# Kernel optimization log

Hardware: AMD Instinct MI355X
Metric: run time of the kernel (lower is better)

The kernel has to match this reference:

```python
import jax, jax.numpy as jnp
import numpy as np
from jax import lax

T, H, I, E = 1024, 1024, 512, 16          # tokens, hidden, moe_intermediate, n_routed_experts
TOP_K, N_GROUP, TOPK_GROUP = 4, 4, 2
N_SHARED = 2
I_SHARED = I * N_SHARED                    # shared-expert intermediate size
ROUTED_SCALE = 2.5


def setup_inputs() -> dict:
    key = jax.random.key(0)
    ks = jax.random.split(key, 9)
    s = lambda k, shape, fan: jax.random.normal(k, shape, jnp.float32) * (fan ** -0.5)
    return {
        "hidden_states": jax.random.normal(ks[0], (T, H), jnp.float32),
        "router_w": s(ks[1], (H, E), H),                 # gate: ReplicatedLinear(H, E)
        "e_bias": jax.random.normal(ks[2], (E,), jnp.float32) * 0.01,  # e_score_correction_bias
        "w_gate": s(ks[3], (E, H, I), H),                # routed experts gate_proj
        "w_up": s(ks[4], (E, H, I), H),                  # routed experts up_proj
        "w_down": s(ks[5], (E, I, H), I),                # routed experts down_proj
        "sw_gate": s(ks[6], (H, I_SHARED), H),           # shared experts gate_proj
        "sw_up": s(ks[7], (H, I_SHARED), H),             # shared experts up_proj
        "sw_down": s(ks[8], (I_SHARED, H), I_SHARED),    # shared experts down_proj
    }


def _grouped_topk_sigmoid(logits, e_bias):
    # DeepSeek-V3 'noaux_tc' grouped top-k with sigmoid scoring.
    scores = jax.nn.sigmoid(logits)                      # [T, E]
    sc = scores + e_bias                                 # biased scores for selection only
    g = sc.reshape(-1, N_GROUP, E // N_GROUP)
    group_scores = lax.top_k(g, 2)[0].sum(-1)            # [T, n_group]: sum of top-2 per group
    _, gidx = lax.top_k(group_scores, TOPK_GROUP)        # [T, topk_group]
    gmask = jax.nn.one_hot(gidx, N_GROUP, dtype=sc.dtype).sum(1)  # [T, n_group]
    emask = jnp.repeat(gmask, E // N_GROUP, axis=1)      # [T, E]
    masked = jnp.where(emask > 0, sc, 0.0)               # sigmoid scores are >=0
    _, tidx = lax.top_k(masked, TOP_K)                   # [T, top_k]
    w = jnp.take_along_axis(scores, tidx, axis=1)        # weights use UNbiased scores
    w = w / (w.sum(-1, keepdims=True) + 1e-20)           # norm_topk_prob=True
    # dense combine weights [T, E]
    combine = (jax.nn.one_hot(tidx, E, dtype=w.dtype) * w[..., None]).sum(1)
    return combine


def reference(hidden_states, router_w, e_bias, w_gate, w_up, w_down,
              sw_gate, sw_up, sw_down):
    x = hidden_states                                    # [T, H]
    logits = x @ router_w                                # [T, E]
    combine = _grouped_topk_sigmoid(logits, e_bias)      # [T, E]

    # routed experts: SiLU-gated MLP per expert, dense-over-experts reference
    gp = jnp.einsum('th,ehi->tei', x, w_gate)            # [T, E, I]
    up = jnp.einsum('th,ehi->tei', x, w_up)
    h = jax.nn.silu(gp) * up
    oe = jnp.einsum('tei,eih->teh', h, w_down)           # [T, E, H]
    routed = jnp.einsum('teh,te->th', oe, combine)       # [T, H]

    # shared experts MLP (reduce_results=False path), fp32 path scales routed only
    shared = (jax.nn.silu(x @ sw_gate) * (x @ sw_up)) @ sw_down  # [T, H]
    return routed * ROUTED_SCALE + shared
```

## Files before the change

### kernel.cpp

```cpp
#include <hip/hip_runtime.h>
#include <stdint.h>

#define T_TOK 1024
#define HDIM  1024
#define IDIM  512
#define NEXP  16
#define ISH   1024
#define MAXT128  48
#define HSLOTS   6144
#define NSCHED   (MAXT128 * 8)

typedef _Float16 f16;
typedef __attribute__((ext_vector_type(8))) _Float16 f16x8;
typedef __attribute__((ext_vector_type(4))) _Float16 f16x4;
typedef __attribute__((ext_vector_type(4))) float    f32x4;

__device__ __forceinline__ void gld16(const void* g, void* l) {
  __builtin_amdgcn_global_load_lds(
      (__attribute__((address_space(1))) void*)(uintptr_t)g,
      (__attribute__((address_space(3))) void*)(uint32_t)(uintptr_t)l,
      16, 0, 0);
}

__device__ __forceinline__ f16x8 ldsfragA(const f16* buf, int row, int lch) {
  int phys = lch ^ (row & 7);
  return *(const f16x8*)(buf + row * 64 + phys * 8);
}

__device__ __forceinline__ f16x8 ldsfragB(const f16* buf, int n, int kc) {
  int c = kc ^ ((n >> 3) & 7);
  return *(const f16x8*)(buf + n * 72 + c * 8);
}

__device__ __forceinline__ void loadB(const float* __restrict__ W, int ldW,
                                      int kt, int n0, int tid2, float2* v) {
  int p = tid2 & 31, kg = tid2 >> 5;
  const float* src = W + (size_t)(kt + 8 * kg) * ldW + n0 + 2 * p;
#pragma unroll
  for (int r = 0; r < 8; r++) v[r] = *(const float2*)(src + (size_t)r * ldW);
}
__device__ __forceinline__ void writeB(f16* __restrict__ Bs, int nbase, int tid2,
                                       const float2* v) {
  int p = tid2 & 31, kg = tid2 >> 5;
  f16x8 c0, c1;
#pragma unroll
  for (int r = 0; r < 8; r++) { c0[r] = (f16)v[r].x; c1[r] = (f16)v[r].y; }
  int nn = nbase + 2 * p;
  int cc = kg ^ ((nn >> 3) & 7);
  *(f16x8*)(Bs + (size_t)nn * 72 + cc * 8) = c0;
  *(f16x8*)(Bs + (size_t)(nn + 1) * 72 + cc * 8) = c1;
}

__global__ __launch_bounds__(256) void router_kernel(
    const float* __restrict__ x, const float* __restrict__ rw, const float* __restrict__ ebias,
    f16* __restrict__ xh, int* __restrict__ topk_i, float* __restrict__ topk_w) {
  int wave = threadIdx.x >> 6, l = threadIdx.x & 63;
  int t = blockIdx.x * 4 + wave;
  float acc[16];
#pragma unroll
  for (int e = 0; e < 16; e++) acc[e] = 0.f;
#pragma unroll
  for (int i = 0; i < 4; i++) {
    int k = i * 256 + l * 4;
    float4 xv = *(const float4*)(x + (size_t)t * HDIM + k);
    f16x4 h = { (f16)xv.x, (f16)xv.y, (f16)xv.z, (f16)xv.w };
    *(f16x4*)(xh + (size_t)t * HDIM + k) = h;
    const float* xp = &xv.x;
#pragma unroll
    for (int j = 0; j < 4; j++) {
      float xj = xp[j];
      const float4* w4 = (const float4*)(rw + (size_t)(k + j) * 16);
#pragma unroll
      for (int q = 0; q < 4; q++) {
        float4 w = w4[q];
        acc[q*4+0] += xj * w.x; acc[q*4+1] += xj * w.y;
        acc[q*4+2] += xj * w.z; acc[q*4+3] += xj * w.w;
      }
    }
  }
#pragma unroll
  for (int off = 32; off >= 1; off >>= 1)
#pragma unroll
    for (int e = 0; e < 16; e++) acc[e] += __shfl_xor(acc[e], off, 64);

  if (l == 0) {
    float s[16], sc[16];
#pragma unroll
    for (int e = 0; e < 16; e++) {
      s[e] = 1.f / (1.f + __expf(-acc[e]));
      sc[e] = s[e] + ebias[e];
    }
    float gs[4];
#pragma unroll
    for (int g = 0; g < 4; g++) {
      float a = -1e30f, b2 = -1e30f;
#pragma unroll
      for (int j = 0; j < 4; j++) {
        float v = sc[g*4 + j];
        if (v > a) { b2 = a; a = v; } else if (v > b2) { b2 = v; }
      }
      gs[g] = a + b2;
    }
    int g1 = 0;
    for (int g = 1; g < 4; g++) if (gs[g] > gs[g1]) g1 = g;
    int g2 = -1;
    for (int g = 0; g < 4; g++) if (g != g1 && (g2 < 0 || gs[g] > gs[g2])) g2 = g;
    float masked[16];
#pragma unroll
    for (int e = 0; e < 16; e++) {
      int g = e >> 2;
      masked[e] = (g == g1 || g == g2) ? sc[e] : 0.0f;
    }
    int idx[4]; float wv[4]; float denom = 1e-20f;
#pragma unroll
    for (int j = 0; j < 4; j++) {
      int best = 0; float bv = masked[0];
      for (int e = 1; e < 16; e++) if (masked[e] > bv) { bv = masked[e]; best = e; }
      idx[j] = best; wv[j] = s[best]; denom += s[best];
      masked[best] = -1e30f;
    }
#pragma unroll
    for (int j = 0; j < 4; j++) {
      topk_i[t * 4 + j] = idx[j];
      topk_w[t * 4 + j] = wv[j] / denom * 2.5f;
    }
  }
}

__global__ __launch_bounds__(1024) void scatter_kernel(
    const int* __restrict__ tki,
    int* __restrict__ tok, int* __restrict__ slotmap,
    int* __restrict__ tile_e, int* __restrict__ tile_srow,
    int* __restrict__ tile_hb, int* __restrict__ ntl, int* __restrict__ sched) {
  __shared__ int lcnt[NEXP], lpos[NEXP], lbase[NEXP];
  int t = threadIdx.x;
  if (t < NEXP) { lcnt[t] = 0; lpos[t] = 0; }
  if (t < NSCHED) sched[t] = -1;
  __syncthreads();
  int idx[4];
#pragma unroll
  for (int j = 0; j < 4; j++) idx[j] = tki[t*4+j];
#pragma unroll
  for (int j = 0; j < 4; j++) atomicAdd(&lcnt[idx[j]], 1);
  __syncthreads();
  if (t == 0) {
    int total = 0, slots = 0;
    int sc[8];
    for (int q = 0; q < 8; q++) sc[q] = 0;
    for (int e = 0; e < NEXP; e++) {
      int c = lcnt[e], nt = (c + 127) >> 7;
      lbase[e] = slots;
      for (int j = 0; j < nt; j++) {
        tile_e[total] = e; tile_srow[total] = j * 128; tile_hb[total] = slots + j * 128;
        int x = e & 7;
        if (sc[x] + 8 > MAXT128) {
          int bx = 0;
          for (int q = 1; q < 8; q++) if (sc[q] < sc[bx]) bx = q;
          x = bx;
        }
        for (int n = 0; n < 8; n++) { sched[x + 8 * sc[x]] = total * 8 + n; sc[x]++; }
        total++;
      }
      slots += nt * 128;
    }
    ntl[0] = total;
  }
  __syncthreads();
#pragma unroll
  for (int j = 0; j < 4; j++) {
    int slot = atomicAdd(&lpos[idx[j]], 1);
    tok[idx[j] * T_TOK + slot] = t;
    slotmap[t * 4 + j] = lbase[idx[j]] + slot;
  }
  __syncthreads();
  int e = t >> 6, s = t & 63;
  int c = lcnt[e];
  int top = ((c + 127) >> 7) << 7;
  for (int s2 = c + s; s2 < top; s2 += 64) tok[e * T_TOK + s2] = 0;
}

__device__ __forceinline__ f32x4 mfma16(f16x8 a, f16x8 b, f32x4 c) {
  return __builtin_amdgcn_mfma_f32_16x16x32_f16(a, b, c, 0, 0, 0);
}

__global__ __launch_bounds__(512, 4) void gu_all(
    const f16* __restrict__ xh,
    const float* __restrict__ sg, const float* __restrict__ su, f16* __restrict__ hsh,
    const float* __restrict__ wg, const float* __restrict__ wu, f16* __restrict__ hbuf,
    const int* __restrict__ tile_e, const int* __restrict__ tile_srow,
    const int* __restrict__ tile_hb, const int* __restrict__ ntl,
    const int* __restrict__ tok, const int* __restrict__ sched) {
  int b = blockIdx.x;
  const float *Bg, *Bu; f16* Hdst;
  int e = 0, srow = 0, mbase, n0, N;
  bool gather = (b >= 128);
  if (!gather) {
    int x = b & 7, s = b >> 3;
    Bg = sg; Bu = su; Hdst = hsh; N = ISH;
    mbase = (s >> 1) * 128;
    n0 = (x + ((s & 1) << 3)) * 64;
  } else {
    int w = sched[b - 128];
    if (w < 0) return;
    int by = w >> 3;
    e = tile_e[by]; srow = tile_srow[by]; mbase = tile_hb[by];
    size_t bo = (size_t)e * HDIM * IDIM;
    Bg = wg + bo; Bu = wu + bo; Hdst = hbuf; N = IDIM;
    n0 = (w & 7) * 64;
  }
  const int K = HDIM;

  __shared__ f16 As[2 * 128 * 64];
  __shared__ f16 Bgs[2 * 64 * 72], Bus[2 * 64 * 72];

  int tid = threadIdx.x, lane = tid & 63, wave = tid >> 6;
  int quad = lane >> 4, l15 = lane & 15;
  int r = lane >> 3, p = lane & 7;

  const f16* gbA[2]; f16* lbA[2];
#pragma unroll
  for (int jj = 0; jj < 2; jj++) {
    int j = wave * 2 + jj;
    int kcol = (p ^ r) << 3;
    int row = j * 8 + r;
    int grow = gather ? tok[e * T_TOK + srow + row] : (mbase + row);
    gbA[jj] = xh + (size_t)grow * K + kcol;
    lbA[jj] = (f16*)As + (j << 9);
  }

  const float* Bmine = (tid < 256) ? Bg : Bu;
  f16* Bsmine = (tid < 256) ? (f16*)Bgs : (f16*)Bus;
  int tid2 = tid & 255;

  int wr = wave >> 1, wc = wave & 1;
  f32x4 zero = {0.f, 0.f, 0.f, 0.f};
  f32x4 aG[2][2], aU[2][2];
#pragma unroll
  for (int mi = 0; mi < 2; mi++)
#pragma unroll
    for (int ni = 0; ni < 2; ni++) { aG[mi][ni] = zero; aU[mi][ni] = zero; }

  float2 v[8];
#pragma unroll
  for (int jj = 0; jj < 2; jj++) gld16(gbA[jj], lbA[jj]);
  loadB(Bmine, N, 0, n0, tid2, v);
  writeB(Bsmine, 0, tid2, v);
  __syncthreads();

  const int nk = K >> 6;
  for (int it = 0; it < nk; ++it) {
    int cb = it & 1, nb = cb ^ 1;
    bool pf = (it + 1 < nk);
    if (pf) {
      int kt = (it + 1) << 6;
#pragma unroll
      for (int jj = 0; jj < 2; jj++) gld16(gbA[jj] + kt, lbA[jj] + nb * 8192);
      loadB(Bmine, N, kt, n0, tid2, v);
    }
    const f16* Ab = (const f16*)As + cb * 8192;
    const f16* Gb = (const f16*)Bgs + cb * 4608;
    const f16* Ub = (const f16*)Bus + cb * 4608;
#pragma unroll
    for (int ks = 0; ks < 2; ks++) {
      int lch = (ks << 2) + quad;
      f16x8 a[2], g[2], u[2];
#pragma unroll
      for (int mi = 0; mi < 2; mi++) a[mi] = ldsfragA(Ab, 32 * wr + 16 * mi + l15, lch);
#pragma unroll
      for (int ni = 0; ni < 2; ni++) {
        g[ni] = ldsfragB(Gb, 32 * wc + 16 * ni + l15, lch);
        u[ni] = ldsfragB(Ub, 32 * wc + 16 * ni + l15, lch);
      }
#pragma unroll
      for (int mi = 0; mi < 2; mi++)
#pragma unroll
        for (int ni = 0; ni < 2; ni++) {
          aG[mi][ni] = mfma16(a[mi], g[ni], aG[mi][ni]);
          aU[mi][ni] = mfma16(a[mi], u[ni], aU[mi][ni]);
        }
    }
    if (pf) writeB(Bsmine + nb * 4608, 0, tid2, v);
    __syncthreads();
  }
#pragma unroll
  for (int mi = 0; mi < 2; mi++)
#pragma unroll
    for (int ni = 0; ni < 2; ni++)
#pragma unroll
      for (int rg = 0; rg < 4; rg++) {
        int m = 32 * wr + 16 * mi + (quad << 2) + rg;
        int n = n0 + 32 * wc + 16 * ni + l15;
        float g = aG[mi][ni][rg], u = aU[mi][ni][rg];
        float val = (g / (1.f + __expf(-g))) * u;
        Hdst[(size_t)(mbase + m) * N + n] = (f16)val;
      }
}

__global__ __launch_bounds__(512, 4) void down_all(
    const f16* __restrict__ hsh, const float* __restrict__ sd,
    const f16* __restrict__ hbuf, const float* __restrict__ wd,
    float* __restrict__ out, f16* __restrict__ odown,
    const int* __restrict__ tile_hb, const int* __restrict__ tile_e,
    const int* __restrict__ ntl, const int* __restrict__ sched) {
  int b = blockIdx.x;
  bool routed = (b >= 64);
  const f16* A; const float* B; int K, abase, n0;
  if (!routed) {
    A = hsh; B = sd; K = ISH;
    n0 = (b & 7) * 128; abase = (b >> 3) * 128;
  } else {
    int w = sched[b - 64];
    if (w < 0) return;
    int by = w >> 3;
    abase = tile_hb[by];
    A = hbuf; B = wd + (size_t)tile_e[by] * IDIM * HDIM; K = IDIM;
    n0 = (w & 7) * 128;
  }

  __shared__ f16 As[2 * 128 * 64];
  __shared__ f16 Bs[2 * 128 * 72];

  int tid = threadIdx.x, lane = tid & 63, wave = tid >> 6;
  int quad = lane >> 4, l15 = lane & 15;
  int r = lane >> 3, p = lane & 7;

  const f16* gbA[2]; f16* lbA[2];
#pragma unroll
  for (int jj = 0; jj < 2; jj++) {
    int j = wave * 2 + jj;
    int kcol = (p ^ r) << 3;
    int row = j * 8 + r;
    gbA[jj] = A + (size_t)(abase + row) * K + kcol;
    lbA[jj] = (f16*)As + (j << 9);
  }

  int nb0 = (tid < 256) ? 0 : 64;
  int tid2 = tid & 255;

  int wr = wave >> 1, wc = wave & 1;
  f32x4 zero = {0.f, 0.f, 0.f, 0.f};
  f32x4 ac[2][4];
#pragma unroll
  for (int mi = 0; mi < 2; mi++)
#pragma unroll
    for (int ni = 0; ni < 4; ni++) ac[mi][ni] = zero;

  float2 v[8];
#pragma unroll
  for (int jj = 0; jj < 2; jj++) gld16(gbA[jj], lbA[jj]);
  loadB(B, HDIM, 0, n0 + nb0, tid2, v);
  writeB((f16*)Bs, nb0, tid2, v);
  __syncthreads();

  const int nk = K >> 6;
  for (int it = 0; it < nk; ++it) {
    int cb = it & 1, nb = cb ^ 1;
    bool pf = (it + 1 < nk);
    if (pf) {
      int kt = (it + 1) << 6;
#pragma unroll
      for (int jj = 0; jj < 2; jj++) gld16(gbA[jj] + kt, lbA[jj] + nb * 8192);
      loadB(B, HDIM, kt, n0 + nb0, tid2, v);
    }
    const f16* Ab = (const f16*)As + cb * 8192;
    const f16* Bb = (const f16*)Bs + cb * 9216;
#pragma unroll
    for (int ks = 0; ks < 2; ks++) {
      int lch = (ks << 2) + quad;
      f16x8 a[2], bb[4];
#pragma unroll
      for (int mi = 0; mi < 2; mi++) a[mi] = ldsfragA(Ab, 32 * wr + 16 * mi + l15, lch);
#pragma unroll
      for (int ni = 0; ni < 4; ni++) bb[ni] = ldsfragB(Bb, 64 * wc + 16 * ni + l15, lch);
#pragma unroll
      for (int mi = 0; mi < 2; mi++)
#pragma unroll
        for (int ni = 0; ni < 4; ni++)
          ac[mi][ni] = mfma16(a[mi], bb[ni], ac[mi][ni]);
    }
    if (pf) writeB((f16*)Bs + nb * 9216, nb0, tid2, v);
    __syncthreads();
  }
#pragma unroll
  for (int mi = 0; mi < 2; mi++)
#pragma unroll
    for (int ni = 0; ni < 4; ni++)
#pragma unroll
      for (int rg = 0; rg < 4; rg++) {
        int m = 32 * wr + 16 * mi + (quad << 2) + rg;
        int n = n0 + 64 * wc + 16 * ni + l15;
        if (routed) odown[(size_t)(abase + m) * HDIM + n] = (f16)ac[mi][ni][rg];
        else        out  [(size_t)(abase + m) * HDIM + n] = ac[mi][ni][rg];
      }
}

__global__ __launch_bounds__(256) void combine_kernel(
    const f16* __restrict__ odown, const int* __restrict__ slotmap,
    const float* __restrict__ tkw, float* __restrict__ out) {
  int t = blockIdx.x;
  __shared__ int ss[4]; __shared__ float sw[4];
  if (threadIdx.x < 4) {
    ss[threadIdx.x] = slotmap[t * 4 + threadIdx.x];
    sw[threadIdx.x] = tkw[t * 4 + threadIdx.x];
  }
  __syncthreads();
  int h = threadIdx.x * 4;
  float4 acc = *(const float4*)(out + (size_t)t * HDIM + h);
#pragma unroll
  for (int j = 0; j < 4; j++) {
    f16x4 v = *(const f16x4*)(odown + (size_t)ss[j] * HDIM + h);
    float wj = sw[j];
    acc.x += wj * (float)v[0]; acc.y += wj * (float)v[1];
    acc.z += wj * (float)v[2]; acc.w += wj * (float)v[3];
  }
  *(float4*)(out + (size_t)t * HDIM + h) = acc;
}

extern "C" void kernel_launch(void* const* d_in, const int* in_sizes, int n_in,
                              void* d_out, int out_size, void* d_ws, size_t ws_size,
                              hipStream_t stream) {
  const float* x  = (const float*)d_in[0];
  const float* rw = (const float*)d_in[1];
  const float* eb = (const float*)d_in[2];
  const float* wg = (const float*)d_in[3];
  const float* wu = (const float*)d_in[4];
  const float* wd = (const float*)d_in[5];
  const float* sg = (const float*)d_in[6];
  const float* su = (const float*)d_in[7];
  const float* sd = (const float*)d_in[8];
  float* out = (float*)d_out;
  (void)in_sizes; (void)n_in; (void)out_size; (void)ws_size;

  char* w = (char*)d_ws;
  size_t off = 0;
  auto alloc = [&](size_t b) { void* p = w + off; off = (off + b + 255) & ~(size_t)255; return p; };

  f16* xh   = (f16*)alloc((size_t)T_TOK * HDIM * 2);
  f16* hbuf = (f16*)alloc((size_t)HSLOTS * IDIM * 2);
  f16* hsh  = (f16*)alloc((size_t)T_TOK * ISH * 2);
  f16* odown = (f16*)alloc((size_t)HSLOTS * HDIM * 2);
  int* topk_i = (int*)alloc((size_t)T_TOK * 4 * 4);
  float* topk_w = (float*)alloc((size_t)T_TOK * 4 * 4);
  int* tok  = (int*)alloc((size_t)NEXP * T_TOK * 4);
  int* slotmap = (int*)alloc((size_t)T_TOK * 4 * 4);
  int* tile_e    = (int*)alloc(MAXT128 * 4);
  int* tile_srow = (int*)alloc(MAXT128 * 4);
  int* tile_hb   = (int*)alloc(MAXT128 * 4);
  int* ntl       = (int*)alloc(16);
  int* sched     = (int*)alloc(NSCHED * 4);

  router_kernel<<<T_TOK / 4, 256, 0, stream>>>(x, rw, eb, xh, topk_i, topk_w);
  scatter_kernel<<<1, 1024, 0, stream>>>(topk_i, tok, slotmap,
                                         tile_e, tile_srow, tile_hb, ntl, sched);
  gu_all<<<128 + NSCHED, 512, 0, stream>>>(
      xh, sg, su, hsh, wg, wu, hbuf, tile_e, tile_srow, tile_hb, ntl, tok, sched);
  down_all<<<64 + NSCHED, 512, 0, stream>>>(
      hsh, sd, hbuf, wd, out, odown, tile_hb, tile_e, ntl, sched);
  combine_kernel<<<T_TOK, 256, 0, stream>>>(odown, slotmap, topk_w, out);
}
```

Baseline: 230.5 us.

## Deepen B-operand register prefetch to two stages with explicit vmcnt waits

Both the gate/up and down GEMM kernels now keep two register buffers for the fp32 B tiles, so the global load for tile t+2 is issued while tile t is computed and tile t+1 is written to LDS. The __syncthreads is replaced by explicit s_waitcnt vmcnt(8) / lgkmcnt(0) plus s_barrier, letting B loads stay in flight across the barrier. The aim is to hide global memory latency of the B weight stream. It adds register pressure from a second float2[8] buffer, and the hand-counted vmcnt assumes a fixed number of outstanding loads per stage, which breaks if the compiler emits a different count.

```diff
diff --git a/kernel.cpp b/kernel.cpp
--- a/kernel.cpp
+++ b/kernel.cpp
@@ -14,6 +14,12 @@
 typedef __attribute__((ext_vector_type(8))) _Float16 f16x8;
 typedef __attribute__((ext_vector_type(4))) _Float16 f16x4;
 typedef __attribute__((ext_vector_type(4))) float    f32x4;
+
+#define CFENCE() asm volatile("" ::: "memory")
+#define VMCNT8() asm volatile("s_waitcnt vmcnt(8)" ::: "memory")
+#define VMCNT0() asm volatile("s_waitcnt vmcnt(0)" ::: "memory")
+#define LGKM0()  asm volatile("s_waitcnt lgkmcnt(0)" ::: "memory")
+#define BARRIER() __builtin_amdgcn_s_barrier()
 
 __device__ __forceinline__ void gld16(const void* g, void* l) {
   __builtin_amdgcn_global_load_lds(
@@ -240,48 +246,71 @@
 #pragma unroll
     for (int ni = 0; ni < 2; ni++) { aG[mi][ni] = zero; aU[mi][ni] = zero; }
 
-  float2 v[8];
+  const int nk = K >> 6;
+  float2 vA[8], vB[8];
+
+  loadB(Bmine, N, 0, n0, tid2, vA);
+  CFENCE();
 #pragma unroll
   for (int jj = 0; jj < 2; jj++) gld16(gbA[jj], lbA[jj]);
-  loadB(Bmine, N, 0, n0, tid2, v);
-  writeB(Bsmine, 0, tid2, v);
-  __syncthreads();
-
-  const int nk = K >> 6;
-  for (int it = 0; it < nk; ++it) {
-    int cb = it & 1, nb = cb ^ 1;
-    bool pf = (it + 1 < nk);
-    if (pf) {
-      int kt = (it + 1) << 6;
-#pragma unroll
-      for (int jj = 0; jj < 2; jj++) gld16(gbA[jj] + kt, lbA[jj] + nb * 8192);
-      loadB(Bmine, N, kt, n0, tid2, v);
-    }
-    const f16* Ab = (const f16*)As + cb * 8192;
-    const f16* Gb = (const f16*)Bgs + cb * 4608;
-    const f16* Ub = (const f16*)Bus + cb * 4608;
-#pragma unroll
-    for (int ks = 0; ks < 2; ks++) {
-      int lch = (ks << 2) + quad;
-      f16x8 a[2], g[2], u[2];
-#pragma unroll
-      for (int mi = 0; mi < 2; mi++) a[mi] = ldsfragA(Ab, 32 * wr + 16 * mi + l15, lch);
-#pragma unroll
-      for (int ni = 0; ni < 2; ni++) {
-        g[ni] = ldsfragB(Gb, 32 * wc + 16 * ni + l15, lch);
-        u[ni] = ldsfragB(Ub, 32 * wc + 16 * ni + l15, lch);
-      }
-#pragma unroll
-      for (int mi = 0; mi < 2; mi++)
-#pragma unroll
-        for (int ni = 0; ni < 2; ni++) {
-          aG[mi][ni] = mfma16(a[mi], g[ni], aG[mi][ni]);
-          aU[mi][ni] = mfma16(a[mi], u[ni], aU[mi][ni]);
-        }
-    }
-    if (pf) writeB(Bsmine + nb * 4608, 0, tid2, v);
-    __syncthreads();
-  }
+  CFENCE();
+  loadB(Bmine, N, 64, n0, tid2, vB);
+  CFENCE();
+  writeB(Bsmine, 0, tid2, vA);
+  VMCNT8();
+  LGKM0();
+  BARRIER();
+
+#define GU_STEP(T, VWR, VLD)                                                  \
+  {                                                                           \
+    const int t_ = (T);                                                       \
+    if (t_ + 1 < nk) {                                                        \
+      int kt = (t_ + 1) << 6, nbuf = (t_ + 1) & 1;                            \
+      gld16(gbA[0] + kt, lbA[0] + nbuf * 8192);                               \
+      gld16(gbA[1] + kt, lbA[1] + nbuf * 8192);                               \
+    }                                                                         \
+    CFENCE();                                                                 \
+    if (t_ + 2 < nk) loadB(Bmine, N, (t_ + 2) << 6, n0, tid2, VLD);           \
+    CFENCE();                                                                 \
+    {                                                                         \
+      const int cb = t_ & 1;                                                  \
+      const f16* Ab = (const f16*)As + cb * 8192;                             \
+      const f16* Gb = (const f16*)Bgs + cb * 4608;                            \
+      const f16* Ub = (const f16*)Bus + cb * 4608;                            \
+      _Pragma("unroll")                                                       \
+      for (int ks = 0; ks < 2; ks++) {                                        \
+        int lch = (ks << 2) + quad;                                           \
+        f16x8 a[2], g[2], u[2];                                               \
+        _Pragma("unroll")                                                     \
+        for (int mi = 0; mi < 2; mi++)                                        \
+          a[mi] = ldsfragA(Ab, 32 * wr + 16 * mi + l15, lch);                 \
+        _Pragma("unroll")                                                     \
+        for (int ni = 0; ni < 2; ni++) {                                      \
+          g[ni] = ldsfragB(Gb, 32 * wc + 16 * ni + l15, lch);                 \
+          u[ni] = ldsfragB(Ub, 32 * wc + 16 * ni + l15, lch);                 \
+        }                                                                     \
+        _Pragma("unroll")                                                     \
+        for (int mi = 0; mi < 2; mi++)                                        \
+          _Pragma("unroll")                                                   \
+          for (int ni = 0; ni < 2; ni++) {                                    \
+            aG[mi][ni] = mfma16(a[mi], g[ni], aG[mi][ni]);                    \
+            aU[mi][ni] = mfma16(a[mi], u[ni], aU[mi][ni]);                    \
+          }                                                                   \
+      }                                                                       \
+    }                                                                         \
+    if (t_ + 1 < nk) writeB(Bsmine + ((t_ + 1) & 1) * 4608, 0, tid2, VWR);    \
+    if (t_ + 2 < nk) { VMCNT8(); }                                            \
+    else if (t_ + 1 < nk) { VMCNT0(); }                                       \
+    LGKM0();                                                                  \
+    BARRIER();                                                                \
+  }
+
+  for (int it = 0; it < nk; it += 2) {
+    GU_STEP(it, vB, vA);
+    GU_STEP(it + 1, vA, vB);
+  }
+#undef GU_STEP
+
 #pragma unroll
   for (int mi = 0; mi < 2; mi++)
 #pragma unroll
@@ -345,42 +374,66 @@
 #pragma unroll
     for (int ni = 0; ni < 4; ni++) ac[mi][ni] = zero;
 
-  float2 v[8];
+  const int nk = K >> 6;
+  float2 vA[8], vB[8];
+
+  loadB(B, HDIM, 0, n0 + nb0, tid2, vA);
+  CFENCE();
 #pragma unroll
   for (int jj = 0; jj < 2; jj++) gld16(gbA[jj], lbA[jj]);
-  loadB(B, HDIM, 0, n0 + nb0, tid2, v);
-  writeB((f16*)Bs, nb0, tid2, v);
-  __syncthreads();
-
-  const int nk = K >> 6;
-  for (int it = 0; it < nk; ++it) {
-    int cb = it & 1, nb = cb ^ 1;
-    bool pf = (it + 1 < nk);
-    if (pf) {
-      int kt = (it + 1) << 6;
-#pragma unroll
-      for (int jj = 0; jj < 2; jj++) gld16(gbA[jj] + kt, lbA[jj] + nb * 8192);
-      loadB(B, HDIM, kt, n0 + nb0, tid2, v);
-    }
-    const f16* Ab = (const f16*)As + cb * 8192;
-    const f16* Bb = (const f16*)Bs + cb * 9216;
-#pragma unroll
-    for (int ks = 0; ks < 2; ks++) {
-      int lch = (ks << 2) + quad;
-      f16x8 a[2], bb[4];
-#pragma unroll
-      for (int mi = 0; mi < 2; mi++) a[mi] = ldsfragA(Ab, 32 * wr + 16 * mi + l15, lch);
-#pragma unroll
-      for (int ni = 0; ni < 4; ni++) bb[ni] = ldsfragB(Bb, 64 * wc + 16 * ni + l15, lch);
-#pragma unroll
-      for (int mi = 0; mi < 2; mi++)
-#pragma unroll
-        for (int ni = 0; ni < 4; ni++)
-          ac[mi][ni] = mfma16(a[mi], bb[ni], ac[mi][ni]);
-    }
-    if (pf) writeB((f16*)Bs + nb * 9216, nb0, tid2, v);
-    __syncthreads();
-  }
+  CFENCE();
+  loadB(B, HDIM, 64, n0 + nb0, tid2, vB);
+  CFENCE();
+  writeB((f16*)Bs, nb0, tid2, vA);
+  VMCNT8();
+  LGKM0();
+  BARRIER();
+
+#define DN_STEP(T, VWR, VLD)                                                  \
+  {                                                                           \
+    const int t_ = (T);                                                       \
+    if (t_ + 1 < nk) {                                                        \
+      int kt = (t_ + 1) << 6, nbuf = (t_ + 1) & 1;                            \
+      gld16(gbA[0] + kt, lbA[0] + nbuf * 8192);                               \
+      gld16(gbA[1] + kt, lbA[1] + nbuf * 8192);                               \
+    }                                                                         \
+    CFENCE();                                                                 \
+    if (t_ + 2 < nk) loadB(B, HDIM, (t_ + 2) << 6, n0 + nb0, tid2, VLD);      \
+    CFENCE();                                                                 \
+    {                                                                         \
+      const int cb = t_ & 1;                                                  \
+      const f16* Ab = (const f16*)As + cb * 8192;                             \
+      const f16* Bb = (const f16*)Bs + cb * 9216;                             \
+      _Pragma("unroll")                                                       \
+      for (int ks = 0; ks < 2; ks++) {                                        \
+        int lch = (ks << 2) + quad;                                           \
+        f16x8 a[2], bb[4];                                                    \
+        _Pragma("unroll")                                                     \
+        for (int mi = 0; mi < 2; mi++)                                        \
+          a[mi] = ldsfragA(Ab, 32 * wr + 16 * mi + l15, lch);                 \
+        _Pragma("unroll")                                                     \
+        for (int ni = 0; ni < 4; ni++)                                        \
+          bb[ni] = ldsfragB(Bb, 64 * wc + 16 * ni + l15, lch);                \
+        _Pragma("unroll")                                                     \
+        for (int mi = 0; mi < 2; mi++)                                        \
+          _Pragma("unroll")                                                   \
+          for (int ni = 0; ni < 4; ni++)                                      \
+            ac[mi][ni] = mfma16(a[mi], bb[ni], ac[mi][ni]);                   \
+      }                                                                       \
+    }                                                                         \
+    if (t_ + 1 < nk) writeB((f16*)Bs + ((t_ + 1) & 1) * 9216, nb0, tid2, VWR);\
+    if (t_ + 2 < nk) { VMCNT8(); }                                            \
+    else if (t_ + 1 < nk) { VMCNT0(); }                                       \
+    LGKM0();                                                                  \
+    BARRIER();                                                                \
+  }
+
+  for (int it = 0; it < nk; it += 2) {
+    DN_STEP(it, vB, vA);
+    DN_STEP(it + 1, vA, vB);
+  }
+#undef DN_STEP
+
 #pragma unroll
   for (int mi = 0; mi < 2; mi++)
 #pragma unroll
```

New measurement: 308.3 us. +33.7%, slower.

## Pre-convert weights to transposed fp16 and load B tiles via direct LDS copies

Applied to the files above, without the earlier changes.

Adds a conversion kernel that transposes all expert and shared weights into fp16 K-contiguous layouts on each call. The gate/up and down GEMMs then stream B tiles with asynchronous global-to-LDS loads using the same swizzle as A, dropping the per-iteration fp32 register loads, conversion and LDS writes. This removes conversion work and halves bytes for repeated weight reads across token tiles. In exchange it adds a full extra pass over all weights (read fp32, write fp16) plus a kernel launch and workspace.

```diff
diff --git a/kernel.cpp b/kernel.cpp
--- a/kernel.cpp
+++ b/kernel.cpp
@@ -9,6 +9,7 @@
 #define MAXT128  48
 #define HSLOTS   6144
 #define NSCHED   (MAXT128 * 8)
+#define NCVT     6912
 
 typedef _Float16 f16;
 typedef __attribute__((ext_vector_type(8))) _Float16 f16x8;
@@ -22,33 +23,57 @@
       16, 0, 0);
 }
 
-__device__ __forceinline__ f16x8 ldsfragA(const f16* buf, int row, int lch) {
+__device__ __forceinline__ f16x8 ldsfrag(const f16* buf, int row, int lch) {
   int phys = lch ^ (row & 7);
   return *(const f16x8*)(buf + row * 64 + phys * 8);
 }
 
-__device__ __forceinline__ f16x8 ldsfragB(const f16* buf, int n, int kc) {
-  int c = kc ^ ((n >> 3) & 7);
-  return *(const f16x8*)(buf + n * 72 + c * 8);
-}
-
-__device__ __forceinline__ void loadB(const float* __restrict__ W, int ldW,
-                                      int kt, int n0, int tid2, float2* v) {
-  int p = tid2 & 31, kg = tid2 >> 5;
-  const float* src = W + (size_t)(kt + 8 * kg) * ldW + n0 + 2 * p;
-#pragma unroll
-  for (int r = 0; r < 8; r++) v[r] = *(const float2*)(src + (size_t)r * ldW);
-}
-__device__ __forceinline__ void writeB(f16* __restrict__ Bs, int nbase, int tid2,
-                                       const float2* v) {
-  int p = tid2 & 31, kg = tid2 >> 5;
-  f16x8 c0, c1;
-#pragma unroll
-  for (int r = 0; r < 8; r++) { c0[r] = (f16)v[r].x; c1[r] = (f16)v[r].y; }
-  int nn = nbase + 2 * p;
-  int cc = kg ^ ((nn >> 3) & 7);
-  *(f16x8*)(Bs + (size_t)nn * 72 + cc * 8) = c0;
-  *(f16x8*)(Bs + (size_t)(nn + 1) * 72 + cc * 8) = c1;
+__global__ __launch_bounds__(256) void cvt_kernel(
+    const float* __restrict__ wg, const float* __restrict__ wu, const float* __restrict__ wd,
+    const float* __restrict__ sg, const float* __restrict__ su, const float* __restrict__ sd,
+    f16* __restrict__ wgt, f16* __restrict__ wut, f16* __restrict__ wdt,
+    f16* __restrict__ sgt, f16* __restrict__ sut, f16* __restrict__ sdt) {
+  int b = blockIdx.x;
+  const float* src; f16* dst; int R, C, tr, tc;
+  if (b < 4096) {
+    int w = b >> 11, e = (b >> 7) & 15, t2 = b & 127;
+    tr = t2 >> 3; tc = t2 & 7;
+    R = 1024; C = 512;
+    src = (w ? wu : wg) + (size_t)e * HDIM * IDIM;
+    dst = (w ? wut : wgt) + (size_t)e * HDIM * IDIM;
+  } else if (b < 6144) {
+    int e = (b - 4096) >> 7, t2 = b & 127;
+    tr = t2 >> 4; tc = t2 & 15;
+    R = 512; C = 1024;
+    src = wd + (size_t)e * HDIM * IDIM;
+    dst = wdt + (size_t)e * HDIM * IDIM;
+  } else {
+    int w = (b - 6144) >> 8, t2 = b & 255;
+    tr = t2 >> 4; tc = t2 & 15;
+    R = 1024; C = 1024;
+    src = (w == 0) ? sg : (w == 1 ? su : sd);
+    dst = (w == 0) ? sgt : (w == 1 ? sut : sdt);
+  }
+  __shared__ f16 tile[64 * 72];
+  int t = threadIdx.x;
+#pragma unroll
+  for (int j = 0; j < 4; j++) {
+    int lin = t + 256 * j;
+    int row = lin >> 4, cc = lin & 15;
+    float4 v = *(const float4*)(src + (size_t)(tr * 64 + row) * C + tc * 64 + cc * 4);
+    f16x4 h = { (f16)v.x, (f16)v.y, (f16)v.z, (f16)v.w };
+    *(f16x4*)(tile + row * 72 + cc * 4) = h;
+  }
+  __syncthreads();
+#pragma unroll
+  for (int j = 0; j < 2; j++) {
+    int lin = t + 256 * j;
+    int n = lin >> 3, c3 = lin & 7;
+    f16x8 o;
+#pragma unroll
+    for (int i = 0; i < 8; i++) o[i] = tile[(c3 * 8 + i) * 72 + n];
+    *(f16x8*)(dst + (size_t)(tc * 64 + n) * R + tr * 64 + c3 * 8) = o;
+  }
 }
 
 __global__ __launch_bounds__(256) void router_kernel(
@@ -185,52 +210,54 @@
 
 __global__ __launch_bounds__(512, 4) void gu_all(
     const f16* __restrict__ xh,
-    const float* __restrict__ sg, const float* __restrict__ su, f16* __restrict__ hsh,
-    const float* __restrict__ wg, const float* __restrict__ wu, f16* __restrict__ hbuf,
+    const f16* __restrict__ sgt, const f16* __restrict__ sut, f16* __restrict__ hsh,
+    const f16* __restrict__ wgt, const f16* __restrict__ wut, f16* __restrict__ hbuf,
     const int* __restrict__ tile_e, const int* __restrict__ tile_srow,
     const int* __restrict__ tile_hb, const int* __restrict__ ntl,
     const int* __restrict__ tok, const int* __restrict__ sched) {
   int b = blockIdx.x;
-  const float *Bg, *Bu; f16* Hdst;
+  const f16 *Bg, *Bu; f16* Hdst;
   int e = 0, srow = 0, mbase, n0, N;
   bool gather = (b >= 128);
   if (!gather) {
     int x = b & 7, s = b >> 3;
-    Bg = sg; Bu = su; Hdst = hsh; N = ISH;
+    Hdst = hsh; N = ISH;
     mbase = (s >> 1) * 128;
     n0 = (x + ((s & 1) << 3)) * 64;
+    Bg = sgt + (size_t)n0 * HDIM; Bu = sut + (size_t)n0 * HDIM;
   } else {
     int w = sched[b - 128];
     if (w < 0) return;
     int by = w >> 3;
     e = tile_e[by]; srow = tile_srow[by]; mbase = tile_hb[by];
-    size_t bo = (size_t)e * HDIM * IDIM;
-    Bg = wg + bo; Bu = wu + bo; Hdst = hbuf; N = IDIM;
+    Hdst = hbuf; N = IDIM;
     n0 = (w & 7) * 64;
+    size_t bo = (size_t)e * HDIM * IDIM + (size_t)n0 * HDIM;
+    Bg = wgt + bo; Bu = wut + bo;
   }
   const int K = HDIM;
 
   __shared__ f16 As[2 * 128 * 64];
-  __shared__ f16 Bgs[2 * 64 * 72], Bus[2 * 64 * 72];
+  __shared__ f16 Bgs[2 * 64 * 64], Bus[2 * 64 * 64];
 
   int tid = threadIdx.x, lane = tid & 63, wave = tid >> 6;
   int quad = lane >> 4, l15 = lane & 15;
   int r = lane >> 3, p = lane & 7;
+  int kcol = (p ^ r) << 3;
 
   const f16* gbA[2]; f16* lbA[2];
 #pragma unroll
   for (int jj = 0; jj < 2; jj++) {
     int j = wave * 2 + jj;
-    int kcol = (p ^ r) << 3;
     int row = j * 8 + r;
     int grow = gather ? tok[e * T_TOK + srow + row] : (mbase + row);
     gbA[jj] = xh + (size_t)grow * K + kcol;
     lbA[jj] = (f16*)As + (j << 9);
   }
-
-  const float* Bmine = (tid < 256) ? Bg : Bu;
-  f16* Bsmine = (tid < 256) ? (f16*)Bgs : (f16*)Bus;
-  int tid2 = tid & 255;
+  const f16* gbBg = Bg + (size_t)(wave * 8 + r) * K + kcol;
+  const f16* gbBu = Bu + (size_t)(wave * 8 + r) * K + kcol;
+  f16* lbBg = (f16*)Bgs + (wave << 9);
+  f16* lbBu = (f16*)Bus + (wave << 9);
 
   int wr = wave >> 1, wc = wave & 1;
   f32x4 zero = {0.f, 0.f, 0.f, 0.f};
@@ -240,36 +267,35 @@
 #pragma unroll
     for (int ni = 0; ni < 2; ni++) { aG[mi][ni] = zero; aU[mi][ni] = zero; }
 
-  float2 v[8];
 #pragma unroll
   for (int jj = 0; jj < 2; jj++) gld16(gbA[jj], lbA[jj]);
-  loadB(Bmine, N, 0, n0, tid2, v);
-  writeB(Bsmine, 0, tid2, v);
+  gld16(gbBg, lbBg);
+  gld16(gbBu, lbBu);
   __syncthreads();
 
   const int nk = K >> 6;
   for (int it = 0; it < nk; ++it) {
     int cb = it & 1, nb = cb ^ 1;
-    bool pf = (it + 1 < nk);
-    if (pf) {
+    if (it + 1 < nk) {
       int kt = (it + 1) << 6;
 #pragma unroll
       for (int jj = 0; jj < 2; jj++) gld16(gbA[jj] + kt, lbA[jj] + nb * 8192);
-      loadB(Bmine, N, kt, n0, tid2, v);
+      gld16(gbBg + kt, lbBg + nb * 4096);
+      gld16(gbBu + kt, lbBu + nb * 4096);
     }
     const f16* Ab = (const f16*)As + cb * 8192;
-    const f16* Gb = (const f16*)Bgs + cb * 4608;
-    const f16* Ub = (const f16*)Bus + cb * 4608;
+    const f16* Gb = (const f16*)Bgs + cb * 4096;
+    const f16* Ub = (const f16*)Bus + cb * 4096;
 #pragma unroll
     for (int ks = 0; ks < 2; ks++) {
       int lch = (ks << 2) + quad;
       f16x8 a[2], g[2], u[2];
 #pragma unroll
-      for (int mi = 0; mi < 2; mi++) a[mi] = ldsfragA(Ab, 32 * wr + 16 * mi + l15, lch);
+      for (int mi = 0; mi < 2; mi++) a[mi] = ldsfrag(Ab, 32 * wr + 16 * mi + l15, lch);
 #pragma unroll
       for (int ni = 0; ni < 2; ni++) {
-        g[ni] = ldsfragB(Gb, 32 * wc + 16 * ni + l15, lch);
-        u[ni] = ldsfragB(Ub, 32 * wc + 16 * ni + l15, lch);
+        g[ni] = ldsfrag(Gb, 32 * wc + 16 * ni + l15, lch);
+        u[ni] = ldsfrag(Ub, 32 * wc + 16 * ni + l15, lch);
       }
 #pragma unroll
       for (int mi = 0; mi < 2; mi++)
@@ -279,7 +305,6 @@
           aU[mi][ni] = mfma16(a[mi], u[ni], aU[mi][ni]);
         }
     }
-    if (pf) writeB(Bsmine + nb * 4608, 0, tid2, v);
     __syncthreads();
   }
 #pragma unroll
@@ -297,45 +322,47 @@
 }
 
 __global__ __launch_bounds__(512, 4) void down_all(
-    const f16* __restrict__ hsh, const float* __restrict__ sd,
-    const f16* __restrict__ hbuf, const float* __restrict__ wd,
+    const f16* __restrict__ hsh, const f16* __restrict__ sdt,
+    const f16* __restrict__ hbuf, const f16* __restrict__ wdt,
     float* __restrict__ out, f16* __restrict__ odown,
     const int* __restrict__ tile_hb, const int* __restrict__ tile_e,
     const int* __restrict__ ntl, const int* __restrict__ sched) {
   int b = blockIdx.x;
   bool routed = (b >= 64);
-  const f16* A; const float* B; int K, abase, n0;
+  const f16* A; const f16* B; int K, abase, n0;
   if (!routed) {
-    A = hsh; B = sd; K = ISH;
+    A = hsh; K = ISH;
     n0 = (b & 7) * 128; abase = (b >> 3) * 128;
+    B = sdt + (size_t)n0 * K;
   } else {
     int w = sched[b - 64];
     if (w < 0) return;
     int by = w >> 3;
     abase = tile_hb[by];
-    A = hbuf; B = wd + (size_t)tile_e[by] * IDIM * HDIM; K = IDIM;
+    A = hbuf; K = IDIM;
     n0 = (w & 7) * 128;
+    B = wdt + (size_t)tile_e[by] * IDIM * HDIM + (size_t)n0 * K;
   }
 
   __shared__ f16 As[2 * 128 * 64];
-  __shared__ f16 Bs[2 * 128 * 72];
+  __shared__ f16 Bs[2 * 128 * 64];
 
   int tid = threadIdx.x, lane = tid & 63, wave = tid >> 6;
   int quad = lane >> 4, l15 = lane & 15;
   int r = lane >> 3, p = lane & 7;
+  int kcol = (p ^ r) << 3;
 
   const f16* gbA[2]; f16* lbA[2];
+  const f16* gbB[2]; f16* lbB[2];
 #pragma unroll
   for (int jj = 0; jj < 2; jj++) {
     int j = wave * 2 + jj;
-    int kcol = (p ^ r) << 3;
     int row = j * 8 + r;
     gbA[jj] = A + (size_t)(abase + row) * K + kcol;
     lbA[jj] = (f16*)As + (j << 9);
-  }
-
-  int nb0 = (tid < 256) ? 0 : 64;
-  int tid2 = tid & 255;
+    gbB[jj] = B + (size_t)row * K + kcol;
+    lbB[jj] = (f16*)Bs + (j << 9);
+  }
 
   int wr = wave >> 1, wc = wave & 1;
   f32x4 zero = {0.f, 0.f, 0.f, 0.f};
@@ -345,40 +372,37 @@
 #pragma unroll
     for (int ni = 0; ni < 4; ni++) ac[mi][ni] = zero;
 
-  float2 v[8];
-#pragma unroll
-  for (int jj = 0; jj < 2; jj++) gld16(gbA[jj], lbA[jj]);
-  loadB(B, HDIM, 0, n0 + nb0, tid2, v);
-  writeB((f16*)Bs, nb0, tid2, v);
+#pragma unroll
+  for (int jj = 0; jj < 2; jj++) { gld16(gbA[jj], lbA[jj]); gld16(gbB[jj], lbB[jj]); }
   __syncthreads();
 
   const int nk = K >> 6;
   for (int it = 0; it < nk; ++it) {
     int cb = it & 1, nb = cb ^ 1;
-    bool pf = (it + 1 < nk);
-    if (pf) {
+    if (it + 1 < nk) {
       int kt = (it + 1) << 6;
 #pragma unroll
-      for (int jj = 0; jj < 2; jj++) gld16(gbA[jj] + kt, lbA[jj] + nb * 8192);
-      loadB(B, HDIM, kt, n0 + nb0, tid2, v);
+      for (int jj = 0; jj < 2; jj++) {
+        gld16(gbA[jj] + kt, lbA[jj] + nb * 8192);
+        gld16(gbB[jj] + kt, lbB[jj] + nb * 8192);
+      }
     }
     const f16* Ab = (const f16*)As + cb * 8192;
-    const f16* Bb = (const f16*)Bs + cb * 9216;
+    const f16* Bb = (const f16*)Bs + cb * 8192;
 #pragma unroll
     for (int ks = 0; ks < 2; ks++) {
       int lch = (ks << 2) + quad;
       f16x8 a[2], bb[4];
 #pragma unroll
-      for (int mi = 0; mi < 2; mi++) a[mi] = ldsfragA(Ab, 32 * wr + 16 * mi + l15, lch);
-#pragma unroll
-      for (int ni = 0; ni < 4; ni++) bb[ni] = ldsfragB(Bb, 64 * wc + 16 * ni + l15, lch);
+      for (int mi = 0; mi < 2; mi++) a[mi] = ldsfrag(Ab, 32 * wr + 16 * mi + l15, lch);
+#pragma unroll
+      for (int ni = 0; ni < 4; ni++) bb[ni] = ldsfrag(Bb, 64 * wc + 16 * ni + l15, lch);
 #pragma unroll
       for (int mi = 0; mi < 2; mi++)
 #pragma unroll
         for (int ni = 0; ni < 4; ni++)
           ac[mi][ni] = mfma16(a[mi], bb[ni], ac[mi][ni]);
     }
-    if (pf) writeB((f16*)Bs + nb * 9216, nb0, tid2, v);
     __syncthreads();
   }
 #pragma unroll
@@ -439,6 +463,12 @@
   f16* hbuf = (f16*)alloc((size_t)HSLOTS * IDIM * 2);
   f16* hsh  = (f16*)alloc((size_t)T_TOK * ISH * 2);
   f16* odown = (f16*)alloc((size_t)HSLOTS * HDIM * 2);
+  f16* wgt  = (f16*)alloc((size_t)NEXP * HDIM * IDIM * 2);
+  f16* wut  = (f16*)alloc((size_t)NEXP * HDIM * IDIM * 2);
+  f16* wdt  = (f16*)alloc((size_t)NEXP * HDIM * IDIM * 2);
+  f16* sgt  = (f16*)alloc((size_t)HDIM * ISH * 2);
+  f16* sut  = (f16*)alloc((size_t)HDIM * ISH * 2);
+  f16* sdt  = (f16*)alloc((size_t)HDIM * ISH * 2);
   int* topk_i = (int*)alloc((size_t)T_TOK * 4 * 4);
   float* topk_w = (float*)alloc((size_t)T_TOK * 4 * 4);
   int* tok  = (int*)alloc((size_t)NEXP * T_TOK * 4);
@@ -449,12 +479,14 @@
   int* ntl       = (int*)alloc(16);
   int* sched     = (int*)alloc(NSCHED * 4);
 
+  cvt_kernel<<<NCVT, 256, 0, stream>>>(wg, wu, wd, sg, su, sd,
+                                       wgt, wut, wdt, sgt, sut, sdt);
   router_kernel<<<T_TOK / 4, 256, 0, stream>>>(x, rw, eb, xh, topk_i, topk_w);
   scatter_kernel<<<1, 1024, 0, stream>>>(topk_i, tok, slotmap,
                                          tile_e, tile_srow, tile_hb, ntl, sched);
   gu_all<<<128 + NSCHED, 512, 0, stream>>>(
-      xh, sg, su, hsh, wg, wu, hbuf, tile_e, tile_srow, tile_hb, ntl, tok, sched);
+      xh, sgt, sut, hsh, wgt, wut, hbuf, tile_e, tile_srow, tile_hb, ntl, tok, sched);
   down_all<<<64 + NSCHED, 512, 0, stream>>>(
-      hsh, sd, hbuf, wd, out, odown, tile_hb, tile_e, ntl, sched);
+      hsh, sdt, hbuf, wdt, out, odown, tile_hb, tile_e, ntl, sched);
   combine_kernel<<<T_TOK, 256, 0, stream>>>(odown, slotmap, topk_w, out);
 }
```

Measured after the change: 227.7 us. Within noise of the previous version (-1.3%).
